# Performance work log

Measured on AMD Instinct MI355X. Metric: run time of the kernel, lower is better.

## Reference

```python
import jax, jax.numpy as jnp
import numpy as np

MARGIN = 0.3


def setup_inputs() -> dict:
    key = jax.random.key(0)
    k1, k2 = jax.random.split(key)
    embeddings = jax.random.normal(k1, (4096, 128), dtype=jnp.float32)
    labels = jax.random.randint(k2, (4096,), 0, 256, dtype=jnp.int64)
    return {"embeddings": embeddings, "labels": labels}


def reference(embeddings, labels):
    # L2-normalize rows (same as F.normalize(p=2, dim=1), eps=1e-12)
    norm = jnp.maximum(jnp.linalg.norm(embeddings, axis=1, keepdims=True), 1e-12)
    e = embeddings / norm
    # cosine distance matrix [N, N]
    dist = 1.0 - e @ e.T

    same = labels[None, :] == labels[:, None]          # [N, N]
    n = labels.shape[0]
    eye = jnp.eye(n, dtype=bool)
    pos_mask = same & ~eye                             # positives excl. self
    neg_mask = ~same

    # dist in [0, 2]; finite sentinels keep max/min well-defined per row
    hardest_pos = jnp.max(jnp.where(pos_mask, dist, -1.0), axis=1)
    hardest_neg = jnp.min(jnp.where(neg_mask, dist, 3.0), axis=1)

    valid = jnp.any(pos_mask, axis=1) & jnp.any(neg_mask, axis=1)
    per_row = jax.nn.relu(hardest_pos - hardest_neg + MARGIN)
    loss_sum = jnp.sum(jnp.where(valid, per_row, 0.0))
    count = jnp.sum(valid)
    return loss_sum / jnp.maximum(count, 1).astype(loss_sum.dtype)
```

## Files before the change

### kernel.cpp

```cpp
#include <hip/hip_runtime.h>
#include <stdint.h>

typedef __bf16 bf16x8 __attribute__((ext_vector_type(8)));
typedef float f32x4 __attribute__((ext_vector_type(4)));

#define N_ROWS 4096
#define KD 128
#define BM 64
#define NCHUNK 32
#define CHUNK 128
#define NBLOCKS (64 * NCHUNK)

#define ENC_POS2 0xC0000000u
#define ENC_NEG2 0x3FFFFFFFu

__device__ __forceinline__ unsigned enc_f32(float f) {
    union { float f; unsigned u; } v; v.f = f;
    return (v.u & 0x80000000u) ? ~v.u : (v.u | 0x80000000u);
}
__device__ __forceinline__ float dec_f32(unsigned e) {
    union { float f; unsigned u; } v;
    v.u = (e & 0x80000000u) ? (e ^ 0x80000000u) : ~e;
    return v.f;
}

__device__ __forceinline__ unsigned short f32_to_bf16_rne(float f) {
    union { float f; uint32_t u; } v; v.f = f;
    uint32_t u = v.u;
    return (unsigned short)((u + 0x7FFFu + ((u >> 16) & 1u)) >> 16);
}

__device__ __forceinline__ int swz(int row, int c) { return row * 16 + (c ^ (row & 15)); }
__device__ __forceinline__ int swzL(int L) { return (L & ~15) | ((L & 15) ^ ((L >> 4) & 15)); }

__global__ __launch_bounds__(256) void normalize_kernel(const float* __restrict__ E,
                                                        unsigned short* __restrict__ out,
                                                        unsigned* __restrict__ hp,
                                                        unsigned* __restrict__ hn,
                                                        unsigned* __restrict__ ticket) {
    const int r0 = blockIdx.x * 4;
    if (threadIdx.x < 4) {
        hp[r0 + threadIdx.x] = ENC_POS2;
        hn[r0 + threadIdx.x] = ENC_NEG2;
    }
    if (blockIdx.x == 0 && threadIdx.x == 0) *ticket = 0u;

    const int wave = threadIdx.x >> 6;
    const int lane = threadIdx.x & 63;
    const int row = r0 + wave;
    const float2 v = *(const float2*)&E[row * KD + lane * 2];
    float s = v.x * v.x + v.y * v.y;
#pragma unroll
    for (int m = 1; m < 64; m <<= 1) s += __shfl_xor(s, m, 64);
    float inv = 0.0f;
    if (s > 0.0f) {
        inv = rsqrtf(s);
        inv = inv * (1.5f - 0.5f * s * inv * inv);
    }
    const unsigned short a = f32_to_bf16_rne(v.x * inv);
    const unsigned short b = f32_to_bf16_rne(v.y * inv);
    ((uint32_t*)out)[row * (KD / 2) + lane] = ((uint32_t)b << 16) | a;
}

__global__ __launch_bounds__(256) void gram_kernel(const unsigned short* __restrict__ Ebits,
                                                   const int* __restrict__ labels,
                                                   unsigned* __restrict__ hp,
                                                   unsigned* __restrict__ hn,
                                                   unsigned* __restrict__ ticket,
                                                   float* __restrict__ out) {
    __shared__ uint4 Bs4[CHUNK * (KD / 8)];
    __shared__ int ljs[CHUNK];
    __shared__ unsigned s_old;
    __shared__ float ssum[4];
    __shared__ int scnt[4];

    const int tid = threadIdx.x;
    const int itile = blockIdx.x & 63;
    const int chunk = blockIdx.x >> 6;
    const int ibase = itile * BM;
    const int cbase = chunk * CHUNK;

    const int wave = tid >> 6, lane = tid & 63;
    const int quad = lane >> 4, l15 = lane & 15;
    const int igb = ibase + wave * 16 + quad * 4;

    {
        const uint4* src = (const uint4*)(Ebits + (size_t)cbase * KD);
#pragma unroll
        for (int it = 0; it < 8; ++it) {
            const int L = it * 256 + tid;
            Bs4[swzL(L)] = src[L];
        }
    }
    if (tid < CHUNK) ljs[tid] = labels[cbase + tid];

    bf16x8 afrag[4];
    {
        const uint4* asrc = (const uint4*)Ebits;
        const int arow = ibase + wave * 16 + l15;
#pragma unroll
        for (int s = 0; s < 4; ++s) afrag[s] = *(const bf16x8*)&asrc[arow * 16 + s * 4 + quad];
    }
    int li_lab[4];
#pragma unroll
    for (int r = 0; r < 4; ++r) li_lab[r] = labels[igb + r];

    __syncthreads();

    float minpos[4] = {2.0f, 2.0f, 2.0f, 2.0f};
    float maxneg[4] = {-2.0f, -2.0f, -2.0f, -2.0f};

#pragma unroll
    for (int t = 0; t < 8; ++t) {
        f32x4 acc = {0.f, 0.f, 0.f, 0.f};
#pragma unroll
        for (int s = 0; s < 4; ++s) {
            const bf16x8 bfrag = *(const bf16x8*)&Bs4[swz(t * 16 + l15, s * 4 + quad)];
            acc = __builtin_amdgcn_mfma_f32_16x16x32_bf16(afrag[s], bfrag, acc, 0, 0, 0);
        }
        const int jg = cbase + t * 16 + l15;
        const int lj = ljs[t * 16 + l15];
#pragma unroll
        for (int r = 0; r < 4; ++r) {
            const float d = acc[r];
            const bool same = (lj == li_lab[r]);
            const float dp = (same && (igb + r != jg)) ? d : 2.0f;
            const float dn = same ? -2.0f : d;
            minpos[r] = fminf(minpos[r], dp);
            maxneg[r] = fmaxf(maxneg[r], dn);
        }
    }

#pragma unroll
    for (int m = 1; m < 16; m <<= 1) {
#pragma unroll
        for (int r = 0; r < 4; ++r) {
            minpos[r] = fminf(minpos[r], __shfl_xor(minpos[r], m, 64));
            maxneg[r] = fmaxf(maxneg[r], __shfl_xor(maxneg[r], m, 64));
        }
    }

    if (l15 == 0) {
#pragma unroll
        for (int r = 0; r < 4; ++r) {
            atomicMin(&hp[igb + r], enc_f32(minpos[r]));
            atomicMax(&hn[igb + r], enc_f32(maxneg[r]));
        }
    }

    __syncthreads();
    if (tid == 0) s_old = atomicAdd(ticket, 1u);
    __syncthreads();
    if (s_old != (unsigned)(NBLOCKS - 1)) return;

    float sum = 0.f; int cnt = 0;
#pragma unroll
    for (int k = 0; k < 16; ++k) {
        const int row = k * 256 + tid;
        const unsigned ep = __hip_atomic_load(&hp[row], __ATOMIC_RELAXED, __HIP_MEMORY_SCOPE_AGENT);
        const unsigned en = __hip_atomic_load(&hn[row], __ATOMIC_RELAXED, __HIP_MEMORY_SCOPE_AGENT);
        const float mp = dec_f32(ep);
        const float mn = dec_f32(en);
        if (mp < 1.5f && mn > -1.5f) {
            sum += fmaxf(0.f, mn - mp + 0.3f);
            ++cnt;
        }
    }
#pragma unroll
    for (int m = 1; m < 64; m <<= 1) {
        sum += __shfl_xor(sum, m, 64);
        cnt += __shfl_xor(cnt, m, 64);
    }
    if (lane == 0) { ssum[wave] = sum; scnt[wave] = cnt; }
    __syncthreads();
    if (tid == 0) {
        const float S = ssum[0] + ssum[1] + ssum[2] + ssum[3];
        const int C = scnt[0] + scnt[1] + scnt[2] + scnt[3];
        out[0] = S / (float)(C > 0 ? C : 1);
    }
}

extern "C" void kernel_launch(void* const* d_in, const int* in_sizes, int n_in,
                              void* d_out, int out_size, void* d_ws, size_t ws_size,
                              hipStream_t stream) {
    const float* E = (const float*)d_in[0];
    const int* labels = (const int*)d_in[1];

    unsigned short* ebits = (unsigned short*)d_ws;
    unsigned* hp = (unsigned*)((char*)d_ws + (size_t)N_ROWS * KD * 2);
    unsigned* hn = hp + N_ROWS;
    unsigned* ticket = hn + N_ROWS;
    float* out = (float*)d_out;

    normalize_kernel<<<N_ROWS / 4, 256, 0, stream>>>(E, ebits, hp, hn, ticket);
    gram_kernel<<<NBLOCKS, 256, 0, stream>>>(ebits, labels, hp, hn, ticket, out);
}
```

Baseline: 86.99 us.

## Fuse normalize, gram and finalize into one cooperative kernel with grid syncs

Replaces the two-launch pipeline and its ticket-based last-block reduction with a single cooperative launch of 1024 blocks. The normalize, gram and finalize phases are separated by grid-wide syncs, and each block now processes two column chunks instead of one. This removes one kernel launch and the atomic ticket, at the cost of two grid barriers and halved parallelism per phase. A three-kernel fallback runs if the cooperative launch fails.

```diff
diff --git a/kernel.cpp b/kernel.cpp
--- a/kernel.cpp
+++ b/kernel.cpp
@@ -1,5 +1,8 @@
 #include <hip/hip_runtime.h>
+#include <hip/hip_cooperative_groups.h>
 #include <stdint.h>
+
+namespace cg = cooperative_groups;
 
 typedef __bf16 bf16x8 __attribute__((ext_vector_type(8)));
 typedef float f32x4 __attribute__((ext_vector_type(4)));
@@ -7,9 +10,9 @@
 #define N_ROWS 4096
 #define KD 128
 #define BM 64
+#define CHUNK 128
 #define NCHUNK 32
-#define CHUNK 128
-#define NBLOCKS (64 * NCHUNK)
+#define GRID_FUSED 1024
 
 #define ENC_POS2 0xC0000000u
 #define ENC_NEG2 0x3FFFFFFFu
@@ -33,20 +36,15 @@
 __device__ __forceinline__ int swz(int row, int c) { return row * 16 + (c ^ (row & 15)); }
 __device__ __forceinline__ int swzL(int L) { return (L & ~15) | ((L & 15) ^ ((L >> 4) & 15)); }
 
-__global__ __launch_bounds__(256) void normalize_kernel(const float* __restrict__ E,
-                                                        unsigned short* __restrict__ out,
-                                                        unsigned* __restrict__ hp,
-                                                        unsigned* __restrict__ hn,
-                                                        unsigned* __restrict__ ticket) {
-    const int r0 = blockIdx.x * 4;
-    if (threadIdx.x < 4) {
-        hp[r0 + threadIdx.x] = ENC_POS2;
-        hn[r0 + threadIdx.x] = ENC_NEG2;
-    }
-    if (blockIdx.x == 0 && threadIdx.x == 0) *ticket = 0u;
-
-    const int wave = threadIdx.x >> 6;
-    const int lane = threadIdx.x & 63;
+__device__ __forceinline__ void normalize_rows(const float* __restrict__ E,
+                                               unsigned short* __restrict__ out,
+                                               unsigned* __restrict__ hp,
+                                               unsigned* __restrict__ hn,
+                                               int bid, int tid) {
+    const int r0 = bid * 4;
+    if (tid < 4) { hp[r0 + tid] = ENC_POS2; hn[r0 + tid] = ENC_NEG2; }
+    const int wave = tid >> 6;
+    const int lane = tid & 63;
     const int row = r0 + wave;
     const float2 v = *(const float2*)&E[row * KD + lane * 2];
     float s = v.x * v.x + v.y * v.y;
@@ -62,37 +60,16 @@
     ((uint32_t*)out)[row * (KD / 2) + lane] = ((uint32_t)b << 16) | a;
 }
 
-__global__ __launch_bounds__(256) void gram_kernel(const unsigned short* __restrict__ Ebits,
-                                                   const int* __restrict__ labels,
-                                                   unsigned* __restrict__ hp,
-                                                   unsigned* __restrict__ hn,
-                                                   unsigned* __restrict__ ticket,
-                                                   float* __restrict__ out) {
-    __shared__ uint4 Bs4[CHUNK * (KD / 8)];
-    __shared__ int ljs[CHUNK];
-    __shared__ unsigned s_old;
-    __shared__ float ssum[4];
-    __shared__ int scnt[4];
-
-    const int tid = threadIdx.x;
-    const int itile = blockIdx.x & 63;
-    const int chunk = blockIdx.x >> 6;
+__device__ __forceinline__ void gram_tile(const unsigned short* __restrict__ Ebits,
+                                          const int* __restrict__ labels,
+                                          unsigned* __restrict__ hp,
+                                          unsigned* __restrict__ hn,
+                                          uint4* Bs4, int* ljs,
+                                          int itile, int cpair, int tid) {
     const int ibase = itile * BM;
-    const int cbase = chunk * CHUNK;
-
     const int wave = tid >> 6, lane = tid & 63;
     const int quad = lane >> 4, l15 = lane & 15;
     const int igb = ibase + wave * 16 + quad * 4;
-
-    {
-        const uint4* src = (const uint4*)(Ebits + (size_t)cbase * KD);
-#pragma unroll
-        for (int it = 0; it < 8; ++it) {
-            const int L = it * 256 + tid;
-            Bs4[swzL(L)] = src[L];
-        }
-    }
-    if (tid < CHUNK) ljs[tid] = labels[cbase + tid];
 
     bf16x8 afrag[4];
     {
@@ -105,30 +82,44 @@
 #pragma unroll
     for (int r = 0; r < 4; ++r) li_lab[r] = labels[igb + r];
 
-    __syncthreads();
-
     float minpos[4] = {2.0f, 2.0f, 2.0f, 2.0f};
     float maxneg[4] = {-2.0f, -2.0f, -2.0f, -2.0f};
 
 #pragma unroll
-    for (int t = 0; t < 8; ++t) {
-        f32x4 acc = {0.f, 0.f, 0.f, 0.f};
-#pragma unroll
-        for (int s = 0; s < 4; ++s) {
-            const bf16x8 bfrag = *(const bf16x8*)&Bs4[swz(t * 16 + l15, s * 4 + quad)];
-            acc = __builtin_amdgcn_mfma_f32_16x16x32_bf16(afrag[s], bfrag, acc, 0, 0, 0);
-        }
-        const int jg = cbase + t * 16 + l15;
-        const int lj = ljs[t * 16 + l15];
-#pragma unroll
-        for (int r = 0; r < 4; ++r) {
-            const float d = acc[r];
-            const bool same = (lj == li_lab[r]);
-            const float dp = (same && (igb + r != jg)) ? d : 2.0f;
-            const float dn = same ? -2.0f : d;
-            minpos[r] = fminf(minpos[r], dp);
-            maxneg[r] = fmaxf(maxneg[r], dn);
-        }
+    for (int cc = 0; cc < 2; ++cc) {
+        const int cbase = (cpair * 2 + cc) * CHUNK;
+        {
+            const uint4* src = (const uint4*)(Ebits + (size_t)cbase * KD);
+#pragma unroll
+            for (int it = 0; it < 8; ++it) {
+                const int L = it * 256 + tid;
+                Bs4[swzL(L)] = src[L];
+            }
+        }
+        if (tid < CHUNK) ljs[tid] = labels[cbase + tid];
+        __syncthreads();
+
+#pragma unroll
+        for (int t = 0; t < 8; ++t) {
+            f32x4 acc = {0.f, 0.f, 0.f, 0.f};
+#pragma unroll
+            for (int s = 0; s < 4; ++s) {
+                const bf16x8 bfrag = *(const bf16x8*)&Bs4[swz(t * 16 + l15, s * 4 + quad)];
+                acc = __builtin_amdgcn_mfma_f32_16x16x32_bf16(afrag[s], bfrag, acc, 0, 0, 0);
+            }
+            const int jg = cbase + t * 16 + l15;
+            const int lj = ljs[t * 16 + l15];
+#pragma unroll
+            for (int r = 0; r < 4; ++r) {
+                const float d = acc[r];
+                const bool same = (lj == li_lab[r]);
+                const float dp = (same && (igb + r != jg)) ? d : 2.0f;
+                const float dn = same ? -2.0f : d;
+                minpos[r] = fminf(minpos[r], dp);
+                maxneg[r] = fmaxf(maxneg[r], dn);
+            }
+        }
+        __syncthreads();
     }
 
 #pragma unroll
@@ -139,7 +130,6 @@
             maxneg[r] = fmaxf(maxneg[r], __shfl_xor(maxneg[r], m, 64));
         }
     }
-
     if (l15 == 0) {
 #pragma unroll
         for (int r = 0; r < 4; ++r) {
@@ -147,12 +137,12 @@
             atomicMax(&hn[igb + r], enc_f32(maxneg[r]));
         }
     }
-
-    __syncthreads();
-    if (tid == 0) s_old = atomicAdd(ticket, 1u);
-    __syncthreads();
-    if (s_old != (unsigned)(NBLOCKS - 1)) return;
-
+}
+
+__device__ __forceinline__ void finalize_body(const unsigned* __restrict__ hp,
+                                              const unsigned* __restrict__ hn,
+                                              float* __restrict__ out,
+                                              int tid, float* ssum, int* scnt) {
     float sum = 0.f; int cnt = 0;
 #pragma unroll
     for (int k = 0; k < 16; ++k) {
@@ -171,6 +161,7 @@
         sum += __shfl_xor(sum, m, 64);
         cnt += __shfl_xor(cnt, m, 64);
     }
+    const int wave = tid >> 6, lane = tid & 63;
     if (lane == 0) { ssum[wave] = sum; scnt[wave] = cnt; }
     __syncthreads();
     if (tid == 0) {
@@ -180,6 +171,53 @@
     }
 }
 
+__global__ __launch_bounds__(256, 4) void fused_kernel(const float* __restrict__ E,
+                                                       const int* __restrict__ labels,
+                                                       unsigned short* __restrict__ ebits,
+                                                       unsigned* __restrict__ hp,
+                                                       unsigned* __restrict__ hn,
+                                                       float* __restrict__ out) {
+    __shared__ uint4 Bs4[CHUNK * (KD / 8)];
+    __shared__ int ljs[CHUNK];
+    __shared__ float ssum[4];
+    __shared__ int scnt[4];
+
+    const int tid = threadIdx.x;
+    normalize_rows(E, ebits, hp, hn, blockIdx.x, tid);
+
+    cg::this_grid().sync();
+
+    gram_tile(ebits, labels, hp, hn, Bs4, ljs, blockIdx.x & 63, blockIdx.x >> 6, tid);
+
+    cg::this_grid().sync();
+
+    if (blockIdx.x == 0) finalize_body(hp, hn, out, tid, ssum, scnt);
+}
+
+__global__ __launch_bounds__(256) void normalize_kernel(const float* __restrict__ E,
+                                                        unsigned short* __restrict__ out,
+                                                        unsigned* __restrict__ hp,
+                                                        unsigned* __restrict__ hn) {
+    normalize_rows(E, out, hp, hn, blockIdx.x, threadIdx.x);
+}
+
+__global__ __launch_bounds__(256, 4) void gram_kernel(const unsigned short* __restrict__ Ebits,
+                                                      const int* __restrict__ labels,
+                                                      unsigned* __restrict__ hp,
+                                                      unsigned* __restrict__ hn) {
+    __shared__ uint4 Bs4[CHUNK * (KD / 8)];
+    __shared__ int ljs[CHUNK];
+    gram_tile(Ebits, labels, hp, hn, Bs4, ljs, blockIdx.x & 63, blockIdx.x >> 6, threadIdx.x);
+}
+
+__global__ __launch_bounds__(256) void finalize_kernel(const unsigned* __restrict__ hp,
+                                                       const unsigned* __restrict__ hn,
+                                                       float* __restrict__ out) {
+    __shared__ float ssum[4];
+    __shared__ int scnt[4];
+    finalize_body(hp, hn, out, threadIdx.x, ssum, scnt);
+}
+
 extern "C" void kernel_launch(void* const* d_in, const int* in_sizes, int n_in,
                               void* d_out, int out_size, void* d_ws, size_t ws_size,
                               hipStream_t stream) {
@@ -189,9 +227,17 @@
     unsigned short* ebits = (unsigned short*)d_ws;
     unsigned* hp = (unsigned*)((char*)d_ws + (size_t)N_ROWS * KD * 2);
     unsigned* hn = hp + N_ROWS;
-    unsigned* ticket = hn + N_ROWS;
     float* out = (float*)d_out;
 
-    normalize_kernel<<<N_ROWS / 4, 256, 0, stream>>>(E, ebits, hp, hn, ticket);
-    gram_kernel<<<NBLOCKS, 256, 0, stream>>>(ebits, labels, hp, hn, ticket, out);
-}
+    void* args[] = {(void*)&E, (void*)&labels, (void*)&ebits,
+                    (void*)&hp, (void*)&hn, (void*)&out};
+    hipError_t err = hipLaunchCooperativeKernel((const void*)fused_kernel,
+                                                dim3(GRID_FUSED), dim3(256),
+                                                args, 0, stream);
+    if (err != hipSuccess) {
+        (void)hipGetLastError();
+        normalize_kernel<<<GRID_FUSED, 256, 0, stream>>>(E, ebits, hp, hn);
+        gram_kernel<<<GRID_FUSED, 256, 0, stream>>>(ebits, labels, hp, hn);
+        finalize_kernel<<<1, 256, 0, stream>>>(hp, hn, out);
+    }
+}
```

Measured after the change: 232.9 us. +167.8%, slower.

## Halve gram grid with two chunks per block and hierarchical completion tickets

Applied to the files above, without the earlier changes.

Each gram block now processes two column chunks sequentially, which halves the grid to 1024 blocks and halves the per-row atomicMin/Max traffic. The single global ticket counter becomes 32 group counters plus one top-level counter, to cut contention on the last-block detection. Launch bounds now request 4 blocks per CU. In exchange, each block does serial load-then-compute work with no overlap between the chunk loads and the MFMAs, and there is less parallelism.

```diff
diff --git a/kernel.cpp b/kernel.cpp
--- a/kernel.cpp
+++ b/kernel.cpp
@@ -7,9 +7,9 @@
 #define N_ROWS 4096
 #define KD 128
 #define BM 64
-#define NCHUNK 32
 #define CHUNK 128
-#define NBLOCKS (64 * NCHUNK)
+#define GRID_GRAM 1024
+#define NGROUP 32
 
 #define ENC_POS2 0xC0000000u
 #define ENC_NEG2 0x3FFFFFFFu
@@ -37,13 +37,10 @@
                                                         unsigned short* __restrict__ out,
                                                         unsigned* __restrict__ hp,
                                                         unsigned* __restrict__ hn,
-                                                        unsigned* __restrict__ ticket) {
+                                                        unsigned* __restrict__ tickets) {
     const int r0 = blockIdx.x * 4;
-    if (threadIdx.x < 4) {
-        hp[r0 + threadIdx.x] = ENC_POS2;
-        hn[r0 + threadIdx.x] = ENC_NEG2;
-    }
-    if (blockIdx.x == 0 && threadIdx.x == 0) *ticket = 0u;
+    if (threadIdx.x < 4) { hp[r0 + threadIdx.x] = ENC_POS2; hn[r0 + threadIdx.x] = ENC_NEG2; }
+    if (blockIdx.x == 0 && threadIdx.x < NGROUP + 1) tickets[threadIdx.x] = 0u;
 
     const int wave = threadIdx.x >> 6;
     const int lane = threadIdx.x & 63;
@@ -62,37 +59,26 @@
     ((uint32_t*)out)[row * (KD / 2) + lane] = ((uint32_t)b << 16) | a;
 }
 
-__global__ __launch_bounds__(256) void gram_kernel(const unsigned short* __restrict__ Ebits,
-                                                   const int* __restrict__ labels,
-                                                   unsigned* __restrict__ hp,
-                                                   unsigned* __restrict__ hn,
-                                                   unsigned* __restrict__ ticket,
-                                                   float* __restrict__ out) {
+__global__ __launch_bounds__(256, 4) void gram_kernel(const unsigned short* __restrict__ Ebits,
+                                                      const int* __restrict__ labels,
+                                                      unsigned* __restrict__ hp,
+                                                      unsigned* __restrict__ hn,
+                                                      unsigned* __restrict__ tickets,
+                                                      float* __restrict__ out) {
     __shared__ uint4 Bs4[CHUNK * (KD / 8)];
     __shared__ int ljs[CHUNK];
-    __shared__ unsigned s_old;
+    __shared__ unsigned s_last;
     __shared__ float ssum[4];
     __shared__ int scnt[4];
 
     const int tid = threadIdx.x;
     const int itile = blockIdx.x & 63;
-    const int chunk = blockIdx.x >> 6;
+    const int cpair = blockIdx.x >> 6;
     const int ibase = itile * BM;
-    const int cbase = chunk * CHUNK;
 
     const int wave = tid >> 6, lane = tid & 63;
     const int quad = lane >> 4, l15 = lane & 15;
     const int igb = ibase + wave * 16 + quad * 4;
-
-    {
-        const uint4* src = (const uint4*)(Ebits + (size_t)cbase * KD);
-#pragma unroll
-        for (int it = 0; it < 8; ++it) {
-            const int L = it * 256 + tid;
-            Bs4[swzL(L)] = src[L];
-        }
-    }
-    if (tid < CHUNK) ljs[tid] = labels[cbase + tid];
 
     bf16x8 afrag[4];
     {
@@ -105,30 +91,44 @@
 #pragma unroll
     for (int r = 0; r < 4; ++r) li_lab[r] = labels[igb + r];
 
-    __syncthreads();
-
     float minpos[4] = {2.0f, 2.0f, 2.0f, 2.0f};
     float maxneg[4] = {-2.0f, -2.0f, -2.0f, -2.0f};
 
 #pragma unroll
-    for (int t = 0; t < 8; ++t) {
-        f32x4 acc = {0.f, 0.f, 0.f, 0.f};
-#pragma unroll
-        for (int s = 0; s < 4; ++s) {
-            const bf16x8 bfrag = *(const bf16x8*)&Bs4[swz(t * 16 + l15, s * 4 + quad)];
-            acc = __builtin_amdgcn_mfma_f32_16x16x32_bf16(afrag[s], bfrag, acc, 0, 0, 0);
-        }
-        const int jg = cbase + t * 16 + l15;
-        const int lj = ljs[t * 16 + l15];
-#pragma unroll
-        for (int r = 0; r < 4; ++r) {
-            const float d = acc[r];
-            const bool same = (lj == li_lab[r]);
-            const float dp = (same && (igb + r != jg)) ? d : 2.0f;
-            const float dn = same ? -2.0f : d;
-            minpos[r] = fminf(minpos[r], dp);
-            maxneg[r] = fmaxf(maxneg[r], dn);
-        }
+    for (int cc = 0; cc < 2; ++cc) {
+        const int cbase = (cpair * 2 + cc) * CHUNK;
+        {
+            const uint4* src = (const uint4*)(Ebits + (size_t)cbase * KD);
+#pragma unroll
+            for (int it = 0; it < 8; ++it) {
+                const int L = it * 256 + tid;
+                Bs4[swzL(L)] = src[L];
+            }
+        }
+        if (tid < CHUNK) ljs[tid] = labels[cbase + tid];
+        __syncthreads();
+
+#pragma unroll
+        for (int t = 0; t < 8; ++t) {
+            f32x4 acc = {0.f, 0.f, 0.f, 0.f};
+#pragma unroll
+            for (int s = 0; s < 4; ++s) {
+                const bf16x8 bfrag = *(const bf16x8*)&Bs4[swz(t * 16 + l15, s * 4 + quad)];
+                acc = __builtin_amdgcn_mfma_f32_16x16x32_bf16(afrag[s], bfrag, acc, 0, 0, 0);
+            }
+            const int jg = cbase + t * 16 + l15;
+            const int lj = ljs[t * 16 + l15];
+#pragma unroll
+            for (int r = 0; r < 4; ++r) {
+                const float d = acc[r];
+                const bool same = (lj == li_lab[r]);
+                const float dp = (same && (igb + r != jg)) ? d : 2.0f;
+                const float dn = same ? -2.0f : d;
+                minpos[r] = fminf(minpos[r], dp);
+                maxneg[r] = fmaxf(maxneg[r], dn);
+            }
+        }
+        __syncthreads();
     }
 
 #pragma unroll
@@ -139,7 +139,6 @@
             maxneg[r] = fmaxf(maxneg[r], __shfl_xor(maxneg[r], m, 64));
         }
     }
-
     if (l15 == 0) {
 #pragma unroll
         for (int r = 0; r < 4; ++r) {
@@ -149,10 +148,20 @@
     }
 
     __syncthreads();
-    if (tid == 0) s_old = atomicAdd(ticket, 1u);
+    if (tid == 0) {
+        __threadfence();
+        const unsigned o = atomicAdd(&tickets[blockIdx.x >> 5], 1u);
+        unsigned lastv = 0u;
+        if (o == 31u) {
+            const unsigned o2 = atomicAdd(&tickets[NGROUP], 1u);
+            lastv = (o2 == (unsigned)(NGROUP - 1)) ? 1u : 0u;
+        }
+        s_last = lastv;
+    }
     __syncthreads();
-    if (s_old != (unsigned)(NBLOCKS - 1)) return;
-
+    if (s_last == 0u) return;
+
+    __threadfence();
     float sum = 0.f; int cnt = 0;
 #pragma unroll
     for (int k = 0; k < 16; ++k) {
@@ -189,9 +198,9 @@
     unsigned short* ebits = (unsigned short*)d_ws;
     unsigned* hp = (unsigned*)((char*)d_ws + (size_t)N_ROWS * KD * 2);
     unsigned* hn = hp + N_ROWS;
-    unsigned* ticket = hn + N_ROWS;
+    unsigned* tickets = hn + N_ROWS;
     float* out = (float*)d_out;
 
-    normalize_kernel<<<N_ROWS / 4, 256, 0, stream>>>(E, ebits, hp, hn, ticket);
-    gram_kernel<<<NBLOCKS, 256, 0, stream>>>(ebits, labels, hp, hn, ticket, out);
-}
+    normalize_kernel<<<N_ROWS / 4, 256, 0, stream>>>(E, ebits, hp, hn, tickets);
+    gram_kernel<<<GRID_GRAM, 256, 0, stream>>>(ebits, labels, hp, hn, tickets, out);
+}
```

Measured after the change: 83.17 us. 4.4% less time.
